# Kernel optimization log

Hardware: AMD Instinct MI355X
Metric: run time of the kernel (lower is better)

Reference implementation:

```python
import jax, jax.numpy as jnp
import numpy as np

EMBED_DIM = 256; NUM_HEADS = 8; NUM_LEVELS = 4; NUM_POINTS = 4; FFN_DIM = 1024
SHAPES = [(128, 128), (64, 64), (32, 32), (16, 16)]
LN_EPS = 1e-5


def setup_inputs() -> dict:
    key = jax.random.key(0)
    ks = jax.random.split(key, 12)
    B = 2; C = EMBED_DIM
    Lin = sum(h * w for h, w in SHAPES)
    starts = np.concatenate([[0], np.cumsum([h * w for h, w in SHAPES])[:-1]])
    MLP2 = NUM_HEADS * NUM_LEVELS * NUM_POINTS
    p = lambda k, *s: jax.random.normal(k, s, jnp.float32) * 0.05
    return {
        "src": jax.random.normal(ks[0], (B, Lin, C), jnp.float32),
        "pos": jax.random.normal(ks[1], (B, Lin, C), jnp.float32),
        "reference_points": jax.random.uniform(ks[2], (B, Lin, NUM_LEVELS, 2), jnp.float32),
        "Wv": p(ks[3], C, C), "bv": jnp.zeros((C,), jnp.float32),
        "Wo": p(ks[4], C, MLP2 * 2),
        "bo": jax.random.uniform(ks[5], (MLP2 * 2,), jnp.float32, -2.0, 2.0),
        "Wa": p(ks[6], C, MLP2), "ba": jnp.zeros((MLP2,), jnp.float32),
        "Wout": p(ks[7], C, C), "bout": jnp.zeros((C,), jnp.float32),
        "gamma": jnp.ones((C,), jnp.float32), "beta": jnp.zeros((C,), jnp.float32),
        "W1": p(ks[8], C, FFN_DIM), "b1": jnp.zeros((FFN_DIM,), jnp.float32),
        "W2": p(ks[9], FFN_DIM, C), "b2": jnp.zeros((C,), jnp.float32),
        "spatial_shapes": jnp.array(SHAPES, dtype=jnp.int32),
        "level_start_index": jnp.array(starts, dtype=jnp.int32),
        "padding_mask": jnp.zeros((B, Lin), dtype=bool),
    }


def _layer_norm(x, g, b):
    m = jnp.mean(x, axis=-1, keepdims=True)
    v = jnp.mean((x - m) ** 2, axis=-1, keepdims=True)
    return (x - m) * jax.lax.rsqrt(v + LN_EPS) * g + b


def _bilinear_sample(val, loc, H, W):
    # val: [B, M, H*W, D]; loc: [B, M, Q, P, 2] normalized [0,1] (x, y)
    # matches torch grid_sample(align_corners=False, padding_mode='zeros')
    x = loc[..., 0] * W - 0.5
    y = loc[..., 1] * H - 0.5
    x0 = jnp.floor(x); y0 = jnp.floor(y)
    lx = x - x0; ly = y - y0
    x0 = x0.astype(jnp.int32); y0 = y0.astype(jnp.int32)
    Bm, M, Q, P = x0.shape
    out = jnp.zeros(val.shape[:2] + (Q, P, val.shape[-1]), val.dtype)
    corners = ((0, 0, (1 - lx) * (1 - ly)), (1, 0, lx * (1 - ly)),
               (0, 1, (1 - lx) * ly), (1, 1, lx * ly))
    for dx, dy, w in corners:
        xi = x0 + dx; yi = y0 + dy
        valid = (xi >= 0) & (xi < W) & (yi >= 0) & (yi < H)
        idx = jnp.clip(yi, 0, H - 1) * W + jnp.clip(xi, 0, W - 1)  # [B,M,Q,P]
        g = jnp.take_along_axis(val, idx.reshape(Bm, M, Q * P, 1), axis=2)
        g = g.reshape(Bm, M, Q, P, -1)
        out = out + (w * valid)[..., None] * g
    return out  # [B, M, Q, P, D]


def _forward(src, pos, reference_points, Wv, bv, Wo, bo, Wa, ba, Wout, bout,
             gamma, beta, W1, b1, W2, b2, spatial_shapes, level_start_index,
             padding_mask):
    M, L, P = NUM_HEADS, NUM_LEVELS, NUM_POINTS
    B, Lin, C = src.shape
    D = C // M
    shapes = np.asarray(spatial_shapes)          # static level geometry
    starts = np.asarray(level_start_index)
    query = src + pos
    value = src @ Wv + bv
    value = jnp.where(padding_mask[..., None], 0.0, value)
    value = value.reshape(B, Lin, M, D).transpose(0, 2, 1, 3)  # [B,M,Lin,D]
    Lq = query.shape[1]
    off = (query @ Wo + bo).reshape(B, Lq, M, L, P, 2)
    attn = jax.nn.softmax((query @ Wa + ba).reshape(B, Lq, M, L * P), axis=-1)
    attn = attn.reshape(B, Lq, M, L, P).transpose(0, 2, 1, 3, 4)  # [B,M,Lq,L,P]
    # offset normalizer is (W, H) per level
    normalizer = jnp.stack([spatial_shapes[:, 1], spatial_shapes[:, 0]], -1).astype(src.dtype)
    loc = reference_points[:, :, None, :, None, :] + off / normalizer[None, None, None, :, None, :]
    loc = loc.transpose(0, 2, 1, 3, 4, 5)  # [B,M,Lq,L,P,2]
    out = jnp.zeros((B, Lq, M, D), src.dtype)
    for l in range(L):
        H, W = int(shapes[l, 0]), int(shapes[l, 1])
        s = int(starts[l])
        vl = value[:, :, s:s + H * W, :]
        samp = _bilinear_sample(vl, loc[:, :, :, l], H, W)  # [B,M,Lq,P,D]
        out = out + jnp.einsum('bmqp,bmqpd->bqmd', attn[:, :, :, l], samp)
    src2 = out.reshape(B, Lq, C) @ Wout + bout
    x = _layer_norm(src + src2, gamma, beta)   # residual + norm (dropout is eval identity)
    h = jax.nn.relu(x @ W1 + b1)               # Mlp, no second residual in this module
    return h @ W2 + b2


def reference(src, pos, reference_points, Wv, bv, Wo, bo, Wa, ba, Wout, bout,
              gamma, beta, W1, b1, W2, b2, spatial_shapes, level_start_index,
              padding_mask):
    return _forward(src, pos, reference_points, Wv, bv, Wo, bo, Wa, ba, Wout,
                    bout, gamma, beta, W1, b1, W2, b2, spatial_shapes,
                    level_start_index, padding_mask)
```

## Files before the change

kernel.cpp:

```cpp
#include <hip/hip_runtime.h>
#include <hip/hip_bf16.h>
#include <math.h>

#define B_SZ   2
#define LIN    21760
#define C_DIM  256
#define M_H    8
#define D_H    32
#define NLEV   4
#define NPTS   4
#define FFN    1024
#define NTOK   (B_SZ * LIN)
#define NTILE  (NTOK / 32)
#define NCONV  (NTOK * C_DIM / 4 / 256)
#define LN_EPS 1e-5f

typedef __bf16 bf16;
typedef bf16  bf16x4 __attribute__((ext_vector_type(4)));
typedef bf16  bf16x8 __attribute__((ext_vector_type(8)));
typedef float f32x4  __attribute__((ext_vector_type(4)));

__device__ __constant__ int c_Ht[4] = {128, 64, 32, 16};
__device__ __constant__ int c_Wt[4] = {128, 64, 32, 16};
__device__ __constant__ int c_St[4] = {0, 16384, 20480, 21504};

static __device__ __forceinline__ float bf2f(unsigned short u) {
    union { float f; unsigned int i; } c;
    c.i = ((unsigned int)u) << 16;
    return c.f;
}

__global__ __launch_bounds__(256) void k_prep(const float* __restrict__ src,
                                              const float* __restrict__ pos,
                                              bf16* __restrict__ srcb,
                                              bf16* __restrict__ qb,
                                              const float* __restrict__ Wv,
                                              const float* __restrict__ Wo,
                                              const float* __restrict__ Wa,
                                              const float* __restrict__ Wout,
                                              const float* __restrict__ W1,
                                              const float* __restrict__ W2,
                                              bf16* __restrict__ Wvt,
                                              bf16* __restrict__ Wqt,
                                              bf16* __restrict__ Woutt,
                                              bf16* __restrict__ W1t,
                                              bf16* __restrict__ W2t) {
    __shared__ float tile[32][33];
    const int bid = blockIdx.x;
    if (bid < NCONV) {
        const int i = bid * 256 + threadIdx.x;
        const float4 s4 = ((const float4*)src)[i];
        const float4 p4 = ((const float4*)pos)[i];
        bf16x4 sb, qb4;
        sb.x = (bf16)s4.x; sb.y = (bf16)s4.y; sb.z = (bf16)s4.z; sb.w = (bf16)s4.w;
        qb4.x = (bf16)(s4.x + p4.x); qb4.y = (bf16)(s4.y + p4.y);
        qb4.z = (bf16)(s4.z + p4.z); qb4.w = (bf16)(s4.w + p4.w);
        ((bf16x4*)srcb)[i] = sb;
        ((bf16x4*)qb)[i]   = qb4;
        return;
    }
    int b = bid - NCONV;
    const float* W; bf16* Wt; int K, N, ntn;
    if      (b < 64)  { W = Wv;   Wt = Wvt;           K = 256;  N = 256;  ntn = 8;            }
    else if (b < 128) { W = Wo;   Wt = Wqt;           K = 256;  N = 256;  ntn = 8;  b -= 64;  }
    else if (b < 160) { W = Wa;   Wt = Wqt + 65536;   K = 256;  N = 128;  ntn = 4;  b -= 128; }
    else if (b < 224) { W = Wout; Wt = Woutt;         K = 256;  N = 256;  ntn = 8;  b -= 160; }
    else if (b < 480) { W = W1;   Wt = W1t;           K = 256;  N = 1024; ntn = 32; b -= 224; }
    else              { W = W2;   Wt = W2t;           K = 1024; N = 256;  ntn = 8;  b -= 480; }

    const int bx = b % ntn;
    const int by = b / ntn;
    const int tx = threadIdx.x & 31, ty = threadIdx.x >> 5;
    const int n0 = bx * 32, k0 = by * 32;
#pragma unroll
    for (int i = 0; i < 32; i += 8)
        tile[ty + i][tx] = W[(long)(k0 + ty + i) * N + n0 + tx];
    __syncthreads();
#pragma unroll
    for (int i = 0; i < 32; i += 8)
        Wt[(long)(n0 + ty + i) * K + k0 + tx] = (bf16)tile[tx][ty + i];
}

#define GEMM_PROLOG(Aptr, BID)                                                \
    const int t = threadIdx.x;                                                \
    const int lane = t & 63, w = t >> 6;                                      \
    const int c0 = lane & 15, kg = lane >> 4;                                 \
    const long tok0 = (long)(BID) * 32;                                       \
    {                                                                         \
        const bf16x8* src8 = (const bf16x8*)((Aptr) + tok0 * C_DIM);          \
        bf16x8* dst8 = (bf16x8*)xs;                                           \
        for (int i = t; i < 1024; i += 256)                                   \
            dst8[i ^ ((i >> 5) & 7)] = src8[i];                               \
    }                                                                         \
    __syncthreads();                                                          \
    bf16x8 afr[2][8];                                                         \
    _Pragma("unroll")                                                         \
    for (int mh = 0; mh < 2; ++mh) {                                          \
        const int m = mh * 16 + c0;                                           \
        _Pragma("unroll")                                                     \
        for (int kc = 0; kc < 8; ++kc) {                                      \
            const int chunk = m * 32 + kc * 4 + kg;                           \
            afr[mh][kc] = ((const bf16x8*)xs)[chunk ^ (m & 7)];               \
        }                                                                     \
    }

__global__ __launch_bounds__(256) void k_vq(const bf16* __restrict__ srcb,
                                            const bf16* __restrict__ qbuf,
                                            const bf16* __restrict__ Wvt,
                                            const float* __restrict__ bv,
                                            bf16* __restrict__ value,
                                            const bf16* __restrict__ Wqt,
                                            const float* __restrict__ bo,
                                            const float* __restrict__ ba,
                                            const float* __restrict__ refp,
                                            float* __restrict__ loc,
                                            float* __restrict__ att) {
    __shared__ bf16 xs[32 * 256];
    if (blockIdx.x < NTILE) {
        GEMM_PROLOG(srcb, blockIdx.x)

        const int b = (int)(tok0 / LIN);
        const int qbase = (int)(tok0 - (long)b * LIN);

#pragma unroll
        for (int nt = 0; nt < 4; ++nt) {
            const int n = w * 64 + nt * 16 + c0;
            f32x4 a0 = {0.f, 0.f, 0.f, 0.f};
            f32x4 a1 = {0.f, 0.f, 0.f, 0.f};
            const bf16* wrow = Wvt + (long)n * 256 + kg * 8;
#pragma unroll
            for (int kc = 0; kc < 8; ++kc) {
                const bf16x8 bfr = *(const bf16x8*)(wrow + kc * 32);
                a0 = __builtin_amdgcn_mfma_f32_16x16x32_bf16(afr[0][kc], bfr, a0, 0, 0, 0);
                a1 = __builtin_amdgcn_mfma_f32_16x16x32_bf16(afr[1][kc], bfr, a1, 0, 0, 0);
            }
            const float bb = bv[n];
            const int m = n >> 5, d = n & 31;
            bf16* vb = value + ((long)(b * M_H + m) * LIN) * D_H + d;
#pragma unroll
            for (int r = 0; r < 4; ++r) {
                const int q0 = qbase + kg * 4 + r;
                vb[(long)q0 * D_H]        = (bf16)(a0[r] + bb);
                vb[(long)(q0 + 16) * D_H] = (bf16)(a1[r] + bb);
            }
        }
    } else {
        GEMM_PROLOG(qbuf, blockIdx.x - NTILE)

#pragma unroll
        for (int nt = 0; nt < 6; ++nt) {
            const int n = w * 96 + nt * 16 + c0;
            f32x4 a0 = {0.f, 0.f, 0.f, 0.f};
            f32x4 a1 = {0.f, 0.f, 0.f, 0.f};
            const bf16* wrow = Wqt + (long)n * 256 + kg * 8;
#pragma unroll
            for (int kc = 0; kc < 8; ++kc) {
                const bf16x8 bfr = *(const bf16x8*)(wrow + kc * 32);
                a0 = __builtin_amdgcn_mfma_f32_16x16x32_bf16(afr[0][kc], bfr, a0, 0, 0, 0);
                a1 = __builtin_amdgcn_mfma_f32_16x16x32_bf16(afr[1][kc], bfr, a1, 0, 0, 0);
            }
            if (n < 256) {
                const int l = (n >> 3) & 3;
                const int c = n & 1;
                const float rnorm = 1.f / ((c == 0) ? (float)c_Wt[l] : (float)c_Ht[l]);
                const float bb = bo[n];
#pragma unroll
                for (int r = 0; r < 4; ++r) {
                    const long t0 = tok0 + kg * 4 + r;
                    const long t1 = t0 + 16;
                    loc[t0 * C_DIM + n] = refp[t0 * 8 + l * 2 + c] + (a0[r] + bb) * rnorm;
                    loc[t1 * C_DIM + n] = refp[t1 * 8 + l * 2 + c] + (a1[r] + bb) * rnorm;
                }
            } else {
                const int j = n - 256;
                const float bb = ba[j];
#pragma unroll
                for (int r = 0; r < 4; ++r) {
                    const long t0 = tok0 + kg * 4 + r;
                    att[t0 * 128 + j]        = a0[r] + bb;
                    att[(t0 + 16) * 128 + j] = a1[r] + bb;
                }
            }
        }
    }
}

__global__ __launch_bounds__(256) void k_samp(const unsigned short* __restrict__ value,
                                              const float* __restrict__ loc,
                                              const float* __restrict__ att,
                                              bf16* __restrict__ outb) {
    __shared__ int4   soff[128];
    __shared__ float4 swgt[128];
    const int t = threadIdx.x;
    const long tok = blockIdx.x;

    if (t < 128) {
        const float lg = att[tok * 128 + t];
        float mx = lg;
#pragma unroll
        for (int s = 1; s < 16; s <<= 1) mx = fmaxf(mx, __shfl_xor(mx, s));
        const float e = expf(lg - mx);
        float sm = e;
#pragma unroll
        for (int s = 1; s < 16; s <<= 1) sm += __shfl_xor(sm, s);
        const float a = e / sm;

        const float2 xy = ((const float2*)loc)[tok * 128 + t];
        const int l = (t >> 2) & 3;
        const int H = c_Ht[l], W = c_Wt[l], s0 = c_St[l];
        const float x = fmaf(xy.x, (float)W, -0.5f);
        const float y = fmaf(xy.y, (float)H, -0.5f);
        const float x0f = floorf(x), y0f = floorf(y);
        const float fx = x - x0f, fy = y - y0f;
        const int x0 = (int)x0f, y0 = (int)y0f;

        const int xi0 = min(max(x0, 0), W - 1);
        const int xi1 = min(max(x0 + 1, 0), W - 1);
        const int yi0 = min(max(y0, 0), H - 1);
        const int yi1 = min(max(y0 + 1, 0), H - 1);
        const float mx0 = (x0 >= 0 && x0 < W) ? 1.f : 0.f;
        const float mx1 = (x0 + 1 < W)        ? 1.f : 0.f;
        const float my0 = (y0 >= 0 && y0 < H) ? 1.f : 0.f;
        const float my1 = (y0 + 1 < H)        ? 1.f : 0.f;
        const float gx0 = (1.f - fx) * mx0, gx1 = fx * ((x0 + 1 >= 0) ? mx1 : 0.f);
        const float gy0 = (1.f - fy) * my0, gy1 = fy * ((y0 + 1 >= 0) ? my1 : 0.f);

        const int r0 = (s0 + yi0 * W) * D_H;
        const int r1 = (s0 + yi1 * W) * D_H;
        soff[t] = (int4){r0 + xi0 * D_H, r0 + xi1 * D_H, r1 + xi0 * D_H, r1 + xi1 * D_H};
        swgt[t] = (float4){a * gx0 * gy0, a * gx1 * gy0, a * gx0 * gy1, a * gx1 * gy1};
    }
    __syncthreads();

    const int m = t >> 5, d = t & 31;
    const int b = (int)(tok / LIN);
    const unsigned short* vb = value + ((long)(b * M_H + m)) * LIN * D_H + d;

    float acc = 0.f;
#pragma unroll
    for (int p = 0; p < 16; ++p) {
        const int jj = m * 16 + p;
        const int4   o = soff[jj];
        const float4 wv = swgt[jj];
        acc = fmaf(bf2f(vb[o.x]), wv.x, acc);
        acc = fmaf(bf2f(vb[o.y]), wv.y, acc);
        acc = fmaf(bf2f(vb[o.z]), wv.z, acc);
        acc = fmaf(bf2f(vb[o.w]), wv.w, acc);
    }
    outb[tok * C_DIM + t] = (bf16)acc;
}

__global__ __launch_bounds__(256) void k_post_mfma(const bf16* __restrict__ A,
                                                   const bf16* __restrict__ Bw,
                                                   const float* __restrict__ bout,
                                                   const float* __restrict__ src,
                                                   const float* __restrict__ g_,
                                                   const float* __restrict__ be_,
                                                   bf16* __restrict__ xb) {
    __shared__ bf16 xs[32 * 256];
    __shared__ float yt[32][256];
    GEMM_PROLOG(A, blockIdx.x)

#pragma unroll
    for (int nt = 0; nt < 4; ++nt) {
        const int n = w * 64 + nt * 16 + c0;
        f32x4 a0 = {0.f, 0.f, 0.f, 0.f};
        f32x4 a1 = {0.f, 0.f, 0.f, 0.f};
        const bf16* wrow = Bw + (long)n * 256 + kg * 8;
#pragma unroll
        for (int kc = 0; kc < 8; ++kc) {
            const bf16x8 bfr = *(const bf16x8*)(wrow + kc * 32);
            a0 = __builtin_amdgcn_mfma_f32_16x16x32_bf16(afr[0][kc], bfr, a0, 0, 0, 0);
            a1 = __builtin_amdgcn_mfma_f32_16x16x32_bf16(afr[1][kc], bfr, a1, 0, 0, 0);
        }
        const float bb = bout[n];
#pragma unroll
        for (int r = 0; r < 4; ++r) {
            const int row = kg * 4 + r;
            yt[row][n]      = a0[r] + bb + src[(tok0 + row) * C_DIM + n];
            yt[row + 16][n] = a1[r] + bb + src[(tok0 + row + 16) * C_DIM + n];
        }
    }
    __syncthreads();

    const float4 g4 = ((const float4*)g_)[lane];
    const float4 b4 = ((const float4*)be_)[lane];
#pragma unroll
    for (int rr = 0; rr < 8; ++rr) {
        const int row = w * 8 + rr;
        const float4 y4 = *(const float4*)&yt[row][lane * 4];
        float s1 = y4.x + y4.y + y4.z + y4.w;
        float s2 = y4.x * y4.x + y4.y * y4.y + y4.z * y4.z + y4.w * y4.w;
#pragma unroll
        for (int s = 1; s < 64; s <<= 1) {
            s1 += __shfl_xor(s1, s);
            s2 += __shfl_xor(s2, s);
        }
        const float mean = s1 * (1.f / 256.f);
        const float var  = s2 * (1.f / 256.f) - mean * mean;
        const float inv  = rsqrtf(var + LN_EPS);
        bf16x4 o;
        o.x = (bf16)((y4.x - mean) * inv * g4.x + b4.x);
        o.y = (bf16)((y4.y - mean) * inv * g4.y + b4.y);
        o.z = (bf16)((y4.z - mean) * inv * g4.z + b4.z);
        o.w = (bf16)((y4.w - mean) * inv * g4.w + b4.w);
        *(bf16x4*)(xb + (tok0 + row) * C_DIM + lane * 4) = o;
    }
}

__global__ __launch_bounds__(256, 2) void k_ffn_mfma(const bf16* __restrict__ x,
                                                     const bf16* __restrict__ W1t,
                                                     const float* __restrict__ b1,
                                                     const bf16* __restrict__ W2t,
                                                     const float* __restrict__ b2,
                                                     float* __restrict__ out) {
    __shared__ bf16 hs[64 * 256];
    const int lane = threadIdx.x & 63, w = threadIdx.x >> 6;
    const int c0 = lane & 15, kg = lane >> 4;
    const long tok0 = (long)blockIdx.x * 64;

    bf16x8 afr[4][8];
#pragma unroll
    for (int mh = 0; mh < 4; ++mh) {
        const bf16* arow = x + (tok0 + mh * 16 + c0) * C_DIM + kg * 8;
#pragma unroll
        for (int kc = 0; kc < 8; ++kc)
            afr[mh][kc] = *(const bf16x8*)(arow + kc * 32);
    }

    f32x4 acc[4][4];
#pragma unroll
    for (int mh = 0; mh < 4; ++mh)
#pragma unroll
        for (int nt = 0; nt < 4; ++nt)
            acc[mh][nt] = (f32x4){0.f, 0.f, 0.f, 0.f};

    for (int c = 0; c < 4; ++c) {
        if (c) __syncthreads();

#pragma unroll
        for (int nt = 0; nt < 4; ++nt) {
            const int nl = w * 64 + nt * 16 + c0;
            const int n  = c * 256 + nl;
            f32x4 a[4];
#pragma unroll
            for (int mh = 0; mh < 4; ++mh) a[mh] = (f32x4){0.f, 0.f, 0.f, 0.f};
            const bf16* wrow = W1t + (long)n * 256 + kg * 8;
#pragma unroll
            for (int kc = 0; kc < 8; ++kc) {
                const bf16x8 bfr = *(const bf16x8*)(wrow + kc * 32);
#pragma unroll
                for (int mh = 0; mh < 4; ++mh)
                    a[mh] = __builtin_amdgcn_mfma_f32_16x16x32_bf16(afr[mh][kc], bfr, a[mh], 0, 0, 0);
            }
            const float bb = b1[n];
#pragma unroll
            for (int mh = 0; mh < 4; ++mh) {
#pragma unroll
                for (int r = 0; r < 4; ++r) {
                    const int row = mh * 16 + kg * 4 + r;
                    hs[(row * 256 + nl) ^ ((row & 7) << 3)] = (bf16)fmaxf(a[mh][r] + bb, 0.f);
                }
            }
        }
        __syncthreads();

#pragma unroll
        for (int kc2 = 0; kc2 < 8; ++kc2) {
            const int kl = kc2 * 32 + kg * 8;
            bf16x8 ah[4];
#pragma unroll
            for (int mh = 0; mh < 4; ++mh) {
                const int row = mh * 16 + c0;
                ah[mh] = *(const bf16x8*)&hs[(row * 256 + kl) ^ ((row & 7) << 3)];
            }
#pragma unroll
            for (int nt = 0; nt < 4; ++nt) {
                const int n = w * 64 + nt * 16 + c0;
                const bf16x8 bfr = *(const bf16x8*)(W2t + (long)n * FFN + c * 256 + kl);
#pragma unroll
                for (int mh = 0; mh < 4; ++mh)
                    acc[mh][nt] = __builtin_amdgcn_mfma_f32_16x16x32_bf16(ah[mh], bfr, acc[mh][nt], 0, 0, 0);
            }
        }
    }

#pragma unroll
    for (int nt = 0; nt < 4; ++nt) {
        const int n = w * 64 + nt * 16 + c0;
        const float bb = b2[n];
#pragma unroll
        for (int mh = 0; mh < 4; ++mh) {
#pragma unroll
            for (int r = 0; r < 4; ++r)
                out[(tok0 + mh * 16 + kg * 4 + r) * C_DIM + n] = acc[mh][nt][r] + bb;
        }
    }
}

extern "C" void kernel_launch(void* const* d_in, const int* in_sizes, int n_in,
                              void* d_out, int out_size, void* d_ws, size_t ws_size,
                              hipStream_t stream) {
    const float* src   = (const float*)d_in[0];
    const float* pos   = (const float*)d_in[1];
    const float* refp  = (const float*)d_in[2];
    const float* Wv    = (const float*)d_in[3];
    const float* bv    = (const float*)d_in[4];
    const float* Wo    = (const float*)d_in[5];
    const float* bo    = (const float*)d_in[6];
    const float* Wa    = (const float*)d_in[7];
    const float* ba    = (const float*)d_in[8];
    const float* Wout  = (const float*)d_in[9];
    const float* bout  = (const float*)d_in[10];
    const float* gamma = (const float*)d_in[11];
    const float* beta  = (const float*)d_in[12];
    const float* W1    = (const float*)d_in[13];
    const float* b1    = (const float*)d_in[14];
    const float* W2    = (const float*)d_in[15];
    const float* b2    = (const float*)d_in[16];

    const size_t N256 = (size_t)NTOK * C_DIM;
    bf16*  srcb = (bf16*)d_ws;
    bf16*  qb   = srcb + N256;
    bf16*  val  = qb + N256;
    float* loc  = (float*)(val + N256);
    float* att  = loc + N256;
    bf16*  Wvt  = (bf16*)(att + (size_t)NTOK * 128);
    bf16*  Wqt  = Wvt + 256 * 256;
    bf16*  Woutt= Wqt + 384 * 256;
    bf16*  W1t  = Woutt + 256 * 256;
    bf16*  W2t  = W1t + (size_t)FFN * C_DIM;
    bf16*  outb = srcb;
    bf16*  xb   = qb;

    dim3 blk(256);
    k_prep<<<NCONV + 736, blk, 0, stream>>>(src, pos, srcb, qb,
                                            Wv, Wo, Wa, Wout, W1, W2,
                                            Wvt, Wqt, Woutt, W1t, W2t);
    k_vq  <<<2 * NTILE, blk, 0, stream>>>(srcb, qb, Wvt, bv, val,
                                          Wqt, bo, ba, refp, loc, att);
    k_samp<<<NTOK, blk, 0, stream>>>((const unsigned short*)val, loc, att, outb);
    k_post_mfma<<<NTILE, blk, 0, stream>>>(outb, Woutt, bout, src, gamma, beta, xb);
    k_ffn_mfma <<<NTOK / 64, blk, 0, stream>>>(xb, W1t, b1, W2t, b2, (float*)d_out);
}
```

Before: 493.6 us.

## Retile fused FFN kernel to 32-token blocks with 512-wide hidden chunks

The fused FFN kernel now handles 32 tokens per block instead of 64 and processes the 1024-wide hidden layer in two 512-wide chunks instead of four 256-wide ones. This halves the A-fragment and accumulator register footprint, drops the min-blocks launch bound, and doubles the grid size, aiming for more parallelism and fewer chunk barriers. In exchange each weight fragment loaded from global memory feeds only two MFMAs instead of four, so total weight traffic per token roughly doubles.

```diff
diff --git a/kernel.cpp b/kernel.cpp
--- a/kernel.cpp
+++ b/kernel.cpp
@@ -308,79 +308,70 @@
     }
 }
 
-__global__ __launch_bounds__(256, 2) void k_ffn_mfma(const bf16* __restrict__ x,
-                                                     const bf16* __restrict__ W1t,
-                                                     const float* __restrict__ b1,
-                                                     const bf16* __restrict__ W2t,
-                                                     const float* __restrict__ b2,
-                                                     float* __restrict__ out) {
-    __shared__ bf16 hs[64 * 256];
+__global__ __launch_bounds__(256) void k_ffn_mfma(const bf16* __restrict__ x,
+                                                  const bf16* __restrict__ W1t,
+                                                  const float* __restrict__ b1,
+                                                  const bf16* __restrict__ W2t,
+                                                  const float* __restrict__ b2,
+                                                  float* __restrict__ out) {
+    __shared__ bf16 hs[32 * 512];
     const int lane = threadIdx.x & 63, w = threadIdx.x >> 6;
     const int c0 = lane & 15, kg = lane >> 4;
-    const long tok0 = (long)blockIdx.x * 64;
-
-    bf16x8 afr[4][8];
-#pragma unroll
-    for (int mh = 0; mh < 4; ++mh) {
+    const long tok0 = (long)blockIdx.x * 32;
+
+    bf16x8 afr[2][8];
+#pragma unroll
+    for (int mh = 0; mh < 2; ++mh) {
         const bf16* arow = x + (tok0 + mh * 16 + c0) * C_DIM + kg * 8;
 #pragma unroll
         for (int kc = 0; kc < 8; ++kc)
             afr[mh][kc] = *(const bf16x8*)(arow + kc * 32);
     }
 
-    f32x4 acc[4][4];
-#pragma unroll
-    for (int mh = 0; mh < 4; ++mh)
+    f32x4 acc[2][4];
+#pragma unroll
+    for (int mh = 0; mh < 2; ++mh)
 #pragma unroll
         for (int nt = 0; nt < 4; ++nt)
             acc[mh][nt] = (f32x4){0.f, 0.f, 0.f, 0.f};
 
-    for (int c = 0; c < 4; ++c) {
+    for (int c = 0; c < 2; ++c) {
         if (c) __syncthreads();
 
 #pragma unroll
-        for (int nt = 0; nt < 4; ++nt) {
-            const int nl = w * 64 + nt * 16 + c0;
-            const int n  = c * 256 + nl;
-            f32x4 a[4];
-#pragma unroll
-            for (int mh = 0; mh < 4; ++mh) a[mh] = (f32x4){0.f, 0.f, 0.f, 0.f};
+        for (int nt = 0; nt < 8; ++nt) {
+            const int nl = w * 128 + nt * 16 + c0;
+            const int n  = c * 512 + nl;
+            f32x4 a0 = {0.f, 0.f, 0.f, 0.f};
+            f32x4 a1 = {0.f, 0.f, 0.f, 0.f};
             const bf16* wrow = W1t + (long)n * 256 + kg * 8;
 #pragma unroll
             for (int kc = 0; kc < 8; ++kc) {
                 const bf16x8 bfr = *(const bf16x8*)(wrow + kc * 32);
-#pragma unroll
-                for (int mh = 0; mh < 4; ++mh)
-                    a[mh] = __builtin_amdgcn_mfma_f32_16x16x32_bf16(afr[mh][kc], bfr, a[mh], 0, 0, 0);
+                a0 = __builtin_amdgcn_mfma_f32_16x16x32_bf16(afr[0][kc], bfr, a0, 0, 0, 0);
+                a1 = __builtin_amdgcn_mfma_f32_16x16x32_bf16(afr[1][kc], bfr, a1, 0, 0, 0);
             }
             const float bb = b1[n];
 #pragma unroll
-            for (int mh = 0; mh < 4; ++mh) {
-#pragma unroll
-                for (int r = 0; r < 4; ++r) {
-                    const int row = mh * 16 + kg * 4 + r;
-                    hs[(row * 256 + nl) ^ ((row & 7) << 3)] = (bf16)fmaxf(a[mh][r] + bb, 0.f);
-                }
+            for (int r = 0; r < 4; ++r) {
+                const int row0 = kg * 4 + r;
+                hs[(row0 * 512 + nl)        ^ ((row0 & 7) << 3)] = (bf16)fmaxf(a0[r] + bb, 0.f);
+                hs[((row0 + 16) * 512 + nl) ^ ((row0 & 7) << 3)] = (bf16)fmaxf(a1[r] + bb, 0.f);
             }
         }
         __syncthreads();
 
 #pragma unroll
-        for (int kc2 = 0; kc2 < 8; ++kc2) {
+        for (int kc2 = 0; kc2 < 16; ++kc2) {
             const int kl = kc2 * 32 + kg * 8;
-            bf16x8 ah[4];
-#pragma unroll
-            for (int mh = 0; mh < 4; ++mh) {
-                const int row = mh * 16 + c0;
-                ah[mh] = *(const bf16x8*)&hs[(row * 256 + kl) ^ ((row & 7) << 3)];
-            }
+            const bf16x8 a0 = *(const bf16x8*)&hs[(c0 * 512 + kl)        ^ ((c0 & 7) << 3)];
+            const bf16x8 a1 = *(const bf16x8*)&hs[((c0 + 16) * 512 + kl) ^ ((c0 & 7) << 3)];
 #pragma unroll
             for (int nt = 0; nt < 4; ++nt) {
                 const int n = w * 64 + nt * 16 + c0;
-                const bf16x8 bfr = *(const bf16x8*)(W2t + (long)n * FFN + c * 256 + kl);
-#pragma unroll
-                for (int mh = 0; mh < 4; ++mh)
-                    acc[mh][nt] = __builtin_amdgcn_mfma_f32_16x16x32_bf16(ah[mh], bfr, acc[mh][nt], 0, 0, 0);
+                const bf16x8 bfr = *(const bf16x8*)(W2t + (long)n * FFN + c * 512 + kl);
+                acc[0][nt] = __builtin_amdgcn_mfma_f32_16x16x32_bf16(a0, bfr, acc[0][nt], 0, 0, 0);
+                acc[1][nt] = __builtin_amdgcn_mfma_f32_16x16x32_bf16(a1, bfr, acc[1][nt], 0, 0, 0);
             }
         }
     }
@@ -390,10 +381,9 @@
         const int n = w * 64 + nt * 16 + c0;
         const float bb = b2[n];
 #pragma unroll
-        for (int mh = 0; mh < 4; ++mh) {
-#pragma unroll
-            for (int r = 0; r < 4; ++r)
-                out[(tok0 + mh * 16 + kg * 4 + r) * C_DIM + n] = acc[mh][nt][r] + bb;
+        for (int r = 0; r < 4; ++r) {
+            out[(tok0 + kg * 4 + r) * C_DIM + n]      = acc[0][nt][r] + bb;
+            out[(tok0 + 16 + kg * 4 + r) * C_DIM + n] = acc[1][nt][r] + bb;
         }
     }
 }
@@ -441,5 +431,5 @@
                                           Wqt, bo, ba, refp, loc, att);
     k_samp<<<NTOK, blk, 0, stream>>>((const unsigned short*)val, loc, att, outb);
     k_post_mfma<<<NTILE, blk, 0, stream>>>(outb, Woutt, bout, src, gamma, beta, xb);
-    k_ffn_mfma <<<NTOK / 64, blk, 0, stream>>>(xb, W1t, b1, W2t, b2, (float*)d_out);
-}
+    k_ffn_mfma <<<NTILE, blk, 0, stream>>>(xb, W1t, b1, W2t, b2, (float*)d_out);
+}
```

Result: faster. 443.3 us (-10.2%).
